# Kernel tuning notes

Measured on AMD Instinct MI355X. Metric: run time of the kernel, lower is better.

## Reference

```python
import jax, jax.numpy as jnp
import numpy as np

B, S, D, H, E, P, TOP_K = 8, 4096, 512, 2048, 8, 16, 2


def setup_inputs() -> dict:
    key = jax.random.key(0)
    ks = jax.random.split(key, 7)
    x = jax.random.normal(ks[0], (B, S, D), dtype=jnp.float32)
    pattern_ids = jax.random.randint(ks[1], (B,), 0, P)
    # router params (init per module: std 0.01 content, std 0.1 pattern bias)
    Wr = 0.01 * jax.random.normal(ks[2], (D, E), dtype=jnp.float32)
    Wp = 0.1 * jax.random.normal(ks[3], (P, E), dtype=jnp.float32)
    # per-expert SwiGLU FFN weights (stacked): w1, w3: [E,D,H], w2: [E,H,D]
    W1 = jax.random.normal(ks[4], (E, D, H), dtype=jnp.float32) / np.float32(np.sqrt(D))
    W2 = jax.random.normal(ks[5], (E, H, D), dtype=jnp.float32) / np.float32(np.sqrt(H))
    W3 = jax.random.normal(ks[6], (E, D, H), dtype=jnp.float32) / np.float32(np.sqrt(D))
    return {"x": x, "pattern_ids": pattern_ids, "Wr": Wr, "Wp": Wp, "W1": W1, "W2": W2, "W3": W3}


def reference(x, pattern_ids, Wr, Wp, W1, W2, W3):
    num_experts = W1.shape[0]
    num_patterns = Wp.shape[0]
    # ---- pattern-aware router ----
    # content logits + per-batch pattern bias broadcast over seq
    logits = jnp.einsum('bsd,de->bse', x, Wr) + Wp[pattern_ids][:, None, :]  # [B,S,E]
    top_w, top_i = jax.lax.top_k(logits, TOP_K)           # [B,S,K]
    gates = jax.nn.softmax(top_w, axis=-1)                # softmax over the top-k logits
    # ---- expert dispatch / combine (loop over small fixed expert count) ----
    y = jnp.zeros_like(x)
    for e in range(num_experts):
        # combined gate weight for expert e per token (0 if not selected)
        w_e = jnp.sum(gates * (top_i == e), axis=-1)      # [B,S]
        h = jnp.einsum('bsd,dh->bsh', x, W1[e]) * jax.nn.silu(jnp.einsum('bsd,dh->bsh', x, W3[e]))
        y = y + w_e[..., None] * jnp.einsum('bsh,hd->bsd', h, W2[e])
    # ---- auxiliary losses ----
    probs = jax.nn.softmax(logits, axis=-1)
    router_z_loss = jnp.mean(jnp.square(logits)) * 0.001
    balance_loss = jnp.mean(jnp.square(probs.mean(axis=(0, 1)) - 1.0 / num_experts))
    Pn = jax.nn.softmax(Wp, axis=-1)
    sim = Pn @ Pn.T
    specialization_loss = jnp.mean(sim * (1.0 - jnp.eye(num_patterns, dtype=sim.dtype))) * 0.1
    return (y, router_z_loss, balance_loss, specialization_loss)
```

## Files before the change

### kernel.cpp

```cpp
#include <hip/hip_runtime.h>
#include <hip/hip_bf16.h>
#include <math.h>


#define B_ 8
#define S_ 4096
#define D_ 512
#define H_ 2048
#define HH (H_ / 2)
#define E_ 8
#define P_ 16
#define NTOK (B_ * S_)
#define NPAIR (NTOK * 2)

typedef __bf16 bf16;
typedef __bf16 bf16x8 __attribute__((ext_vector_type(8)));
typedef float f32x4 __attribute__((ext_vector_type(4)));

#define OFF_GATES 256
#define OFF_LIST (OFF_GATES + NPAIR * 4)
#define OFF_XBF (OFF_LIST + E_ * NTOK * 4)
#define OFF_W13T (OFF_XBF + (size_t)NTOK * D_ * 2)
#define OFF_W2T (OFF_W13T + (size_t)E_ * 2 * H_ * D_ * 2)
#define OFF_HBUF (OFF_W2T + (size_t)E_ * D_ * H_ * 2)
#define WS_NEEDED (OFF_HBUF + (size_t)NPAIR * HH * 2)

__device__ __forceinline__ void gl16(const bf16* g, bf16* l) {
  __builtin_amdgcn_global_load_lds((const __attribute__((address_space(1))) unsigned int*)g,
                                   (__attribute__((address_space(3))) unsigned int*)l, 16, 0, 0);
}

__global__ __launch_bounds__(256) void router_kernel(
    const float* __restrict__ x, const int* __restrict__ pids,
    const float* __restrict__ Wr, const float* __restrict__ Wp,
    bf16* __restrict__ xbf, float* __restrict__ gates, int* __restrict__ lists,
    int* __restrict__ counts, float* __restrict__ probSum, float* __restrict__ zSum) {
  __shared__ float xs[32 * 516];
  __shared__ float wr_s[E_ * 516];
  __shared__ float wp_s[E_];
  __shared__ float probAcc[E_];
  __shared__ float zAcc;
  __shared__ int lcnt[E_], lbase[E_];
  __shared__ float lg_s[32][E_ + 1];

  const int tid = threadIdx.x;
  const int tok0 = blockIdx.x * 32;

#pragma unroll
  for (int rep = 0; rep < (D_ * E_) / 256; ++rep) {
    int flat = rep * 256 + tid;
    wr_s[(flat & 7) * 516 + (flat >> 3)] = Wr[flat];
  }
  if (tid < E_) {
    wp_s[tid] = Wp[pids[tok0 >> 12] * E_ + tid];
    probAcc[tid] = 0.f;
    lcnt[tid] = 0;
  }
  if (tid == 0) zAcc = 0.f;

  const float4* x4 = (const float4*)(x + (size_t)tok0 * D_);
#pragma unroll
  for (int rep = 0; rep < 16; ++rep) {
    int idx = rep * 256 + tid;
    float4 v = x4[idx];
    int t = idx >> 7;
    int d = (idx & 127) * 4;
    *(float4*)(xs + t * 516 + d) = v;
    union { unsigned short u[4]; uint2 qq; } pk;
    pk.u[0] = __builtin_bit_cast(unsigned short, (bf16)v.x);
    pk.u[1] = __builtin_bit_cast(unsigned short, (bf16)v.y);
    pk.u[2] = __builtin_bit_cast(unsigned short, (bf16)v.z);
    pk.u[3] = __builtin_bit_cast(unsigned short, (bf16)v.w);
    *(uint2*)(xbf + (size_t)tok0 * D_ + (size_t)idx * 4) = pk.qq;
  }
  __syncthreads();

  const int t = tid >> 3, e = tid & 7;
  const int lane = tid & 63;
  {
    float a0 = 0.f, a1 = 0.f, a2 = 0.f, a3 = 0.f;
    const float* xr = xs + t * 516;
    const float* wr = wr_s + e * 516;
#pragma unroll 8
    for (int d = 0; d < D_; d += 4) {
      float4 xv = *(const float4*)(xr + d);
      float4 wv = *(const float4*)(wr + d);
      a0 += xv.x * wv.x;
      a1 += xv.y * wv.y;
      a2 += xv.z * wv.z;
      a3 += xv.w * wv.w;
    }
    lg_s[t][e] = (a0 + a1) + (a2 + a3) + wp_s[e];
  }
  __syncthreads();

  float v[E_];
#pragma unroll
  for (int k = 0; k < E_; ++k) v[k] = lg_s[t][k];
  const float lg = v[e];
  float m = v[0];
#pragma unroll
  for (int k = 1; k < E_; ++k) m = fmaxf(m, v[k]);
  float s = 0.f;
#pragma unroll
  for (int k = 0; k < E_; ++k) s += expf(v[k] - m);
  float prob = expf(lg - m) / s;
  float z = lg * lg;
  int i1 = 0;
  float v1 = v[0];
#pragma unroll
  for (int k = 1; k < E_; ++k)
    if (v[k] > v1) { v1 = v[k]; i1 = k; }
  int i2 = -1;
  float v2 = -1e30f;
#pragma unroll
  for (int k = 0; k < E_; ++k)
    if (k != i1 && v[k] > v2) { v2 = v[k]; i2 = k; }

  float p = prob;
  p += __shfl_xor(p, 8);
  p += __shfl_xor(p, 16);
  p += __shfl_xor(p, 32);
  float zz = z;
#pragma unroll
  for (int off = 1; off < 64; off <<= 1) zz += __shfl_xor(zz, off);
  if (lane < 8) atomicAdd(&probAcc[e], p);
  if (lane == 0) atomicAdd(&zAcc, zz);

  int r = (e == i1) ? 0 : ((e == i2) ? 1 : -1);
  int pos = -1;
  if (r >= 0) {
    float ex = expf(v2 - v1);
    float g = (r == 0) ? 1.f / (1.f + ex) : ex / (1.f + ex);
    gates[(tok0 + t) * 2 + r] = g;
    pos = atomicAdd(&lcnt[e], 1);
  }
  __syncthreads();
  if (tid < E_) lbase[tid] = atomicAdd(&counts[tid], lcnt[tid]);
  __syncthreads();
  if (r >= 0) lists[e * NTOK + lbase[e] + pos] = (tok0 + t) * 2 + r;
  if (tid < E_) atomicAdd(&probSum[tid], probAcc[tid]);
  else if (tid == 8) atomicAdd(zSum, zAcc);
}

__global__ __launch_bounds__(256) void transpose_convert(const float* __restrict__ in,
                                                         bf16* __restrict__ out, int R, int C,
                                                         size_t out_estride, int mode) {
  const int e = blockIdx.z;
  const int r0 = blockIdx.y * 64, c0 = blockIdx.x * 64;
  in += (size_t)e * R * C;
  out += (size_t)e * out_estride;
  __shared__ unsigned int lt[64 * 33];

  const int tid = threadIdx.x;
  const int m = tid & 15, qq = tid >> 4;
#pragma unroll
  for (int rep = 0; rep < 2; ++rep) {
    int rp = qq + rep * 16;
    const float4 a = *(const float4*)(in + (size_t)(r0 + rp * 2) * C + c0 + m * 4);
    const float4 b = *(const float4*)(in + (size_t)(r0 + rp * 2 + 1) * C + c0 + m * 4);
#pragma unroll
    for (int j = 0; j < 4; ++j) {
      unsigned short lo = __builtin_bit_cast(unsigned short, (bf16)((&a.x)[j]));
      unsigned short hi = __builtin_bit_cast(unsigned short, (bf16)((&b.x)[j]));
      lt[(m * 4 + j) * 33 + rp] = (unsigned int)lo | ((unsigned int)hi << 16);
    }
  }
  __syncthreads();
  const int c = tid >> 2, dw0 = (tid & 3) * 8;
  unsigned int vv[8];
#pragma unroll
  for (int j = 0; j < 8; ++j) vv[j] = lt[c * 33 + dw0 + j];
  int orow = c0 + c;
  if (mode >= 0) orow = ((orow >> 4) << 5) | (orow & 15) | mode;
  uint4* dst = (uint4*)(out + (size_t)orow * R + r0 + dw0 * 2);
  dst[0] = make_uint4(vv[0], vv[1], vv[2], vv[3]);
  dst[1] = make_uint4(vv[4], vv[5], vv[6], vv[7]);
}

__global__ __launch_bounds__(512, 4) void gemm1_kernel(
    const bf16* __restrict__ xbf, const bf16* __restrict__ W13T,
    const int* __restrict__ counts, const int* __restrict__ lists,
    const float* __restrict__ gates, bf16* __restrict__ hbuf, int half) {
  const int e = (int)blockIdx.z;
  const int count = counts[e];
  const int m0 = blockIdx.y * 128;
  if (m0 >= count) return;
  int hbase = 0;
  for (int j = 0; j < e; ++j) hbase += counts[j];
  const int nb = (int)blockIdx.x;
  const int n0 = nb * 256 + half * (2 * HH);
  const int* list_e = lists + e * NTOK;
  const bf16* Be = W13T + (size_t)e * (2 * H_) * D_;

  __shared__ bf16 sA[2 * 128 * 32];
  __shared__ bf16 sB[2 * 256 * 32];
  __shared__ int stok[128];
  __shared__ float sgate[128];

  const int tid = threadIdx.x;
  if (tid < 128) {
    int rg = m0 + tid;
    int pr = (rg < count) ? list_e[rg] : 0;
    stok[tid] = pr >> 1;
    sgate[tid] = (rg < count) ? gates[pr] : 0.f;
  }
  __syncthreads();

  const int wave = tid >> 6, lane = tid & 63;
  const int rsub = lane >> 2, kq = lane & 3;
  const int scol = (kq ^ ((lane >> 3) & 3)) * 8;
  const int rS = wave * 16 + rsub;
  const bf16* aP0 = xbf + (size_t)stok[rS] * D_ + scol;
  const bf16* bP0 = Be + (size_t)(n0 + rS) * D_ + scol;
  const bf16* bP1 = Be + (size_t)(n0 + 128 + rS) * D_ + scol;
  bf16* lA0 = sA + wave * 512;
  bf16* lB0 = sB + wave * 512;
  bf16* lB1 = sB + (wave + 8) * 512;

  const int wm = wave >> 2, wn = wave & 3;
  const int lm = lane & 15, q = lane >> 4;
  const int rq = (q ^ ((lm >> 1) & 3)) * 8;
  const bf16* aRd = sA + (wm * 64 + lm) * 32 + rq;
  const bf16* bRd = sB + (wn * 64 + lm) * 32 + rq;

  f32x4 acc[4][4] = {};

  gl16(aP0, lA0);
  gl16(bP0, lB0);
  gl16(bP1, lB1);
  __syncthreads();

  int cur = 0;
  for (int t = 1; t < D_ / 32; ++t) {
    const int koff = t * 32;
    const int nxtA = (cur ^ 1) * 4096;
    const int nxtB = (cur ^ 1) * 8192;
    gl16(aP0 + koff, lA0 + nxtA);
    gl16(bP0 + koff, lB0 + nxtB);
    gl16(bP1 + koff, lB1 + nxtB);
    const bf16* aR = aRd + cur * 4096;
    const bf16* bR = bRd + cur * 8192;
    bf16x8 af[4], bf_[4];
#pragma unroll
    for (int i = 0; i < 4; ++i) {
      af[i] = *(const bf16x8*)(aR + i * 512);
      bf_[i] = *(const bf16x8*)(bR + i * 512);
    }
#pragma unroll
    for (int mt = 0; mt < 4; ++mt)
#pragma unroll
      for (int nt = 0; nt < 4; ++nt)
        acc[mt][nt] =
            __builtin_amdgcn_mfma_f32_16x16x32_bf16(af[mt], bf_[nt], acc[mt][nt], 0, 0, 0);
    __syncthreads();
    cur ^= 1;
  }
  {
    const bf16* aR = aRd + cur * 4096;
    const bf16* bR = bRd + cur * 8192;
    bf16x8 af[4], bf_[4];
#pragma unroll
    for (int i = 0; i < 4; ++i) {
      af[i] = *(const bf16x8*)(aR + i * 512);
      bf_[i] = *(const bf16x8*)(bR + i * 512);
    }
#pragma unroll
    for (int mt = 0; mt < 4; ++mt)
#pragma unroll
      for (int nt = 0; nt < 4; ++nt)
        acc[mt][nt] =
            __builtin_amdgcn_mfma_f32_16x16x32_bf16(af[mt], bf_[nt], acc[mt][nt], 0, 0, 0);
  }

  const int hb = nb * 128 + wn * 32;
#pragma unroll
  for (int mt = 0; mt < 4; ++mt) {
#pragma unroll
    for (int u = 0; u < 2; ++u) {
#pragma unroll
      for (int r = 0; r < 4; ++r) {
        int lrow = wm * 64 + mt * 16 + q * 4 + r;
        int grow = m0 + lrow;
        if (grow < count) {
          float v1 = acc[mt][2 * u][r];
          float v3 = acc[mt][2 * u + 1][r];
          float g = v1 * (v3 / (1.f + __expf(-v3))) * sgate[lrow];
          hbuf[(size_t)(hbase + grow) * HH + hb + u * 16 + lm] = (bf16)g;
        }
      }
    }
  }
}

__global__ __launch_bounds__(256, 2) void gemm2_kernel(const bf16* __restrict__ hbuf,
                                                       const bf16* __restrict__ W2T,
                                                       const int* __restrict__ counts,
                                                       const int* __restrict__ lists,
                                                       float* __restrict__ y, int half) {
  const int e = (int)blockIdx.z;
  const int count = counts[e];
  const int m0 = blockIdx.y * 128;
  if (m0 >= count) return;
  int hbase = 0;
  for (int j = 0; j < e; ++j) hbase += counts[j];
  const int n0 = blockIdx.x * 128;
  const int kb = half * HH;
  const bf16* W2e = W2T + (size_t)e * D_ * H_;
  const int* list_e = lists + e * NTOK;

  __shared__ bf16 sA[4 * 128 * 32];
  __shared__ bf16 sB[4 * 128 * 32];
  __shared__ int stok[128];

  const int tid = threadIdx.x;
  if (tid < 128) {
    int rg = m0 + tid;
    stok[tid] = (rg < count) ? (list_e[rg] >> 1) : 0;
  }
  __syncthreads();

  const int wave = tid >> 6, lane = tid & 63;
  const int rsub = lane >> 2, kq = lane & 3;
  const int scol = (kq ^ ((lane >> 3) & 3)) * 8;
  const int rA0 = wave * 16 + rsub, rA1 = 64 + wave * 16 + rsub;
  int ra0 = hbase + m0 + rA0;
  int ra1 = hbase + m0 + rA1;
  if (ra0 >= NPAIR) ra0 = NPAIR - 1;
  if (ra1 >= NPAIR) ra1 = NPAIR - 1;
  const bf16* aP0 = hbuf + (size_t)ra0 * HH + scol;
  const bf16* aP1 = hbuf + (size_t)ra1 * HH + scol;
  const bf16* bP0 = W2e + (size_t)(n0 + rA0) * H_ + kb + scol;
  const bf16* bP1 = W2e + (size_t)(n0 + rA1) * H_ + kb + scol;

  const int wm = wave >> 1, wn = wave & 1;
  const int lm = lane & 15, q = lane >> 4;
  const int rq = (q ^ ((lm >> 1) & 3)) * 8;
  const bf16* aRd = sA + (wm * 64 + lm) * 32 + rq;
  const bf16* bRd = sB + (wn * 64 + lm) * 32 + rq;

  f32x4 acc[4][4] = {};

  auto STAGE = [&](int t, int bi) {
    const int ko = t * 32;
    bf16* ba = sA + bi * 4096;
    bf16* bb = sB + bi * 4096;
    gl16(aP0 + ko, ba + wave * 512);
    gl16(aP1 + ko, ba + (wave + 4) * 512);
    gl16(bP0 + ko, bb + wave * 512);
    gl16(bP1 + ko, bb + (wave + 4) * 512);
  };
  auto COMP = [&](int bi) {
    const bf16* aR = aRd + bi * 4096;
    const bf16* bR = bRd + bi * 4096;
    bf16x8 af[4], bf_[4];
#pragma unroll
    for (int i = 0; i < 4; ++i) {
      af[i] = *(const bf16x8*)(aR + i * 512);
      bf_[i] = *(const bf16x8*)(bR + i * 512);
    }
#pragma unroll
    for (int mt = 0; mt < 4; ++mt)
#pragma unroll
      for (int nt = 0; nt < 4; ++nt)
        acc[mt][nt] =
            __builtin_amdgcn_mfma_f32_16x16x32_bf16(af[mt], bf_[nt], acc[mt][nt], 0, 0, 0);
  };

  const int NT = HH / 32;
  STAGE(0, 0);
  STAGE(1, 1);
  for (int t = 0; t < NT - 2; ++t) {
    STAGE(t + 2, (t + 2) & 3);
    asm volatile("s_waitcnt vmcnt(8) lgkmcnt(0)" ::: "memory");
    __builtin_amdgcn_s_barrier();
    COMP(t & 3);
  }
  asm volatile("s_waitcnt vmcnt(4) lgkmcnt(0)" ::: "memory");
  __builtin_amdgcn_s_barrier();
  COMP((NT - 2) & 3);
  asm volatile("s_waitcnt vmcnt(0) lgkmcnt(0)" ::: "memory");
  __builtin_amdgcn_s_barrier();
  COMP((NT - 1) & 3);

#pragma unroll
  for (int mt = 0; mt < 4; ++mt) {
#pragma unroll
    for (int nt = 0; nt < 4; ++nt) {
#pragma unroll
      for (int r = 0; r < 4; ++r) {
        int lrow = wm * 64 + mt * 16 + q * 4 + r;
        int grow = m0 + lrow;
        if (grow < count) {
          atomicAdd(&y[(size_t)stok[lrow] * D_ + n0 + wn * 64 + nt * 16 + lm], acc[mt][nt][r]);
        }
      }
    }
  }
}

__global__ __launch_bounds__(256) void finalize_kernel(const float* __restrict__ Wp,
                                                       const float* __restrict__ probSum,
                                                       const float* __restrict__ zSum,
                                                       float* __restrict__ out) {
  __shared__ float pn[P_][E_];
  __shared__ float simAcc;
  const int tid = threadIdx.x;
  if (tid == 0) simAcc = 0.f;
  if (tid < P_) {
    float v[E_], m = -1e30f, s = 0.f;
#pragma unroll
    for (int e = 0; e < E_; ++e) {
      v[e] = Wp[tid * E_ + e];
      m = fmaxf(m, v[e]);
    }
#pragma unroll
    for (int e = 0; e < E_; ++e) {
      float ex = expf(v[e] - m);
      pn[tid][e] = ex;
      s += ex;
    }
#pragma unroll
    for (int e = 0; e < E_; ++e) pn[tid][e] /= s;
  }
  __syncthreads();
  {
    int i = tid >> 4, j = tid & 15;
    if (i != j) {
      float d = 0.f;
#pragma unroll
      for (int e = 0; e < E_; ++e) d += pn[i][e] * pn[j][e];
      atomicAdd(&simAcc, d);
    }
  }
  __syncthreads();
  if (tid == 0) {
    out[0] = zSum[0] / (float)(NTOK * E_) * 0.001f;
    float bl = 0.f;
#pragma unroll
    for (int e = 0; e < E_; ++e) {
      float pm = probSum[e] / (float)NTOK - 1.f / (float)E_;
      bl += pm * pm;
    }
    out[1] = bl / (float)E_;
    out[2] = simAcc / (float)(P_ * P_) * 0.1f;
  }
}

extern "C" void kernel_launch(void* const* d_in, const int* in_sizes, int n_in, void* d_out,
                              int out_size, void* d_ws, size_t ws_size, hipStream_t stream) {
  const float* x = (const float*)d_in[0];
  const int* pids = (const int*)d_in[1];
  const float* Wr = (const float*)d_in[2];
  const float* Wp = (const float*)d_in[3];
  const float* W1 = (const float*)d_in[4];
  const float* W2 = (const float*)d_in[5];
  const float* W3 = (const float*)d_in[6];
  float* y = (float*)d_out;

  if (ws_size < WS_NEEDED) return;

  char* ws = (char*)d_ws;
  int* counts = (int*)ws;
  float* probSum = (float*)(ws + 32);
  float* zSum = (float*)(ws + 64);
  float* gates = (float*)(ws + OFF_GATES);
  int* lists = (int*)(ws + OFF_LIST);
  bf16* xbf = (bf16*)(ws + OFF_XBF);
  bf16* W13T = (bf16*)(ws + OFF_W13T);
  bf16* W2T = (bf16*)(ws + OFF_W2T);
  bf16* hbuf = (bf16*)(ws + OFF_HBUF);

  hipMemsetAsync(ws, 0, 256, stream);
  hipMemsetAsync(d_out, 0, (size_t)NTOK * D_ * 4, stream);

  router_kernel<<<dim3(NTOK / 32), 256, 0, stream>>>(x, pids, Wr, Wp, xbf, gates, lists, counts,
                                                     probSum, zSum);
  transpose_convert<<<dim3(H_ / 64, D_ / 64, E_), 256, 0, stream>>>(W1, W13T, D_, H_,
                                                                    (size_t)2 * H_ * D_, 0);
  transpose_convert<<<dim3(H_ / 64, D_ / 64, E_), 256, 0, stream>>>(W3, W13T, D_, H_,
                                                                    (size_t)2 * H_ * D_, 16);
  transpose_convert<<<dim3(D_ / 64, H_ / 64, E_), 256, 0, stream>>>(W2, W2T, H_, D_,
                                                                    (size_t)H_ * D_, -1);

  for (int half = 0; half < 2; ++half) {
    gemm1_kernel<<<dim3((2 * HH) / 256, NTOK / 128, E_), 512, 0, stream>>>(
        xbf, W13T, counts, lists, gates, hbuf, half);
    gemm2_kernel<<<dim3(D_ / 128, NTOK / 128, E_), 256, 0, stream>>>(hbuf, W2T, counts, lists,
                                                                     y, half);
  }
  finalize_kernel<<<1, 256, 0, stream>>>(Wp, probSum, zSum, y + (size_t)NTOK * D_);
}
```

Baseline: 962.9 us.

## Keep full A row-block resident in LDS and stream all gemm1 N-chunks per block

gemm1 now loads a 64-token tile of gathered x (the full K=512) into LDS once, with an XOR swizzle. Each block then loops over all N-chunks of the W1/W3 half, double-buffering B tiles and running a SwiGLU epilogue per 256-column chunk. This removes the repeated gather of x rows across many N blocks and the per-block startup costs. The trade-offs are 64 KB of A in LDS, lower occupancy (launch bounds 4→2), and a much smaller grid with x-dimension 1, which may leave CUs underused.

```diff
diff --git a/kernel.cpp b/kernel.cpp
--- a/kernel.cpp
+++ b/kernel.cpp
@@ -178,118 +178,124 @@
   dst[1] = make_uint4(vv[4], vv[5], vv[6], vv[7]);
 }
 
-__global__ __launch_bounds__(512, 4) void gemm1_kernel(
+__global__ __launch_bounds__(512, 2) void gemm1_kernel(
     const bf16* __restrict__ xbf, const bf16* __restrict__ W13T,
     const int* __restrict__ counts, const int* __restrict__ lists,
     const float* __restrict__ gates, bf16* __restrict__ hbuf, int half) {
   const int e = (int)blockIdx.z;
   const int count = counts[e];
-  const int m0 = blockIdx.y * 128;
+  const int m0 = blockIdx.y * 64;
   if (m0 >= count) return;
   int hbase = 0;
   for (int j = 0; j < e; ++j) hbase += counts[j];
-  const int nb = (int)blockIdx.x;
-  const int n0 = nb * 256 + half * (2 * HH);
   const int* list_e = lists + e * NTOK;
   const bf16* Be = W13T + (size_t)e * (2 * H_) * D_;
 
-  __shared__ bf16 sA[2 * 128 * 32];
-  __shared__ bf16 sB[2 * 256 * 32];
-  __shared__ int stok[128];
-  __shared__ float sgate[128];
+  __shared__ bf16 sA[8 * 4096];
+  __shared__ bf16 sB[2 * 512 * 32];
 
   const int tid = threadIdx.x;
-  if (tid < 128) {
-    int rg = m0 + tid;
-    int pr = (rg < count) ? list_e[rg] : 0;
-    stok[tid] = pr >> 1;
-    sgate[tid] = (rg < count) ? gates[pr] : 0.f;
-  }
-  __syncthreads();
-
   const int wave = tid >> 6, lane = tid & 63;
+  const int lm = lane & 15, q = lane >> 4;
+
+  float gte[4][4];
+#pragma unroll
+  for (int mt = 0; mt < 4; ++mt)
+#pragma unroll
+    for (int r = 0; r < 4; ++r) {
+      int grow = m0 + mt * 16 + q * 4 + r;
+      gte[mt][r] = (grow < count) ? gates[list_e[grow]] : 0.f;
+    }
+
+  const int rA = lane >> 3;
+  const int c16 = lane & 7;
+  {
+    int rowA = m0 + wave * 8 + rA;
+    int prA = (rowA < count) ? list_e[rowA] : 0;
+    const bf16* aSrc = xbf + (size_t)(prA >> 1) * D_ + (c16 ^ rA) * 8;
+    bf16* aDst = sA + wave * 4096;
+#pragma unroll
+    for (int j = 0; j < 8; ++j) gl16(aSrc + j * 64, aDst + j * 512);
+  }
+
   const int rsub = lane >> 2, kq = lane & 3;
   const int scol = (kq ^ ((lane >> 3) & 3)) * 8;
-  const int rS = wave * 16 + rsub;
-  const bf16* aP0 = xbf + (size_t)stok[rS] * D_ + scol;
-  const bf16* bP0 = Be + (size_t)(n0 + rS) * D_ + scol;
-  const bf16* bP1 = Be + (size_t)(n0 + 128 + rS) * D_ + scol;
-  bf16* lA0 = sA + wave * 512;
-  bf16* lB0 = sB + wave * 512;
-  bf16* lB1 = sB + (wave + 8) * 512;
-
-  const int wm = wave >> 2, wn = wave & 3;
-  const int lm = lane & 15, q = lane >> 4;
+  const bf16* bPbase =
+      Be + (size_t)(half * (2 * HH) + wave * 64 + rsub) * D_ + scol;
+  auto STAGE_B = [&](int s, int buf) {
+    int c = s >> 4, t = s & 15;
+    size_t off = (size_t)c * 512 * D_ + t * 32;
+    bf16* d = sB + buf * 16384 + wave * 2048;
+#pragma unroll
+    for (int sl = 0; sl < 4; ++sl) gl16(bPbase + off + (size_t)sl * 16 * D_, d + sl * 512);
+  };
+
+  const int r7 = lm & 7;
+  int aStat[4];
+#pragma unroll
+  for (int mt = 0; mt < 4; ++mt)
+    aStat[mt] = (mt * 2 + (lm >> 3)) * 8192 + (lm & 7) * 128;
   const int rq = (q ^ ((lm >> 1) & 3)) * 8;
-  const bf16* aRd = sA + (wm * 64 + lm) * 32 + rq;
-  const bf16* bRd = sB + (wn * 64 + lm) * 32 + rq;
+  const char* aBase = (const char*)sA;
 
   f32x4 acc[4][4] = {};
 
-  gl16(aP0, lA0);
-  gl16(bP0, lB0);
-  gl16(bP1, lB1);
-  __syncthreads();
-
-  int cur = 0;
-  for (int t = 1; t < D_ / 32; ++t) {
-    const int koff = t * 32;
-    const int nxtA = (cur ^ 1) * 4096;
-    const int nxtB = (cur ^ 1) * 8192;
-    gl16(aP0 + koff, lA0 + nxtA);
-    gl16(bP0 + koff, lB0 + nxtB);
-    gl16(bP1 + koff, lB1 + nxtB);
-    const bf16* aR = aRd + cur * 4096;
-    const bf16* bR = bRd + cur * 8192;
+  auto COMP = [&](int s, int buf) {
+    const int t15 = s & 15;
+    const int c64 = (t15 >> 1) * 1024;
+    const int cc = (t15 * 4 + q) & 7;
     bf16x8 af[4], bf_[4];
 #pragma unroll
-    for (int i = 0; i < 4; ++i) {
-      af[i] = *(const bf16x8*)(aR + i * 512);
-      bf_[i] = *(const bf16x8*)(bR + i * 512);
-    }
+    for (int mt = 0; mt < 4; ++mt)
+      af[mt] = *(const bf16x8*)(aBase + aStat[mt] + c64 + ((cc ^ r7) << 4));
+    const bf16* bR = sB + buf * 16384 + (wave * 64 + lm) * 32 + rq;
+#pragma unroll
+    for (int nt = 0; nt < 4; ++nt) bf_[nt] = *(const bf16x8*)(bR + nt * 512);
 #pragma unroll
     for (int mt = 0; mt < 4; ++mt)
 #pragma unroll
       for (int nt = 0; nt < 4; ++nt)
         acc[mt][nt] =
             __builtin_amdgcn_mfma_f32_16x16x32_bf16(af[mt], bf_[nt], acc[mt][nt], 0, 0, 0);
-    __syncthreads();
-    cur ^= 1;
-  }
-  {
-    const bf16* aR = aRd + cur * 4096;
-    const bf16* bR = bRd + cur * 8192;
-    bf16x8 af[4], bf_[4];
-#pragma unroll
-    for (int i = 0; i < 4; ++i) {
-      af[i] = *(const bf16x8*)(aR + i * 512);
-      bf_[i] = *(const bf16x8*)(bR + i * 512);
-    }
-#pragma unroll
-    for (int mt = 0; mt < 4; ++mt)
-#pragma unroll
-      for (int nt = 0; nt < 4; ++nt)
-        acc[mt][nt] =
-            __builtin_amdgcn_mfma_f32_16x16x32_bf16(af[mt], bf_[nt], acc[mt][nt], 0, 0, 0);
-  }
-
-  const int hb = nb * 128 + wn * 32;
-#pragma unroll
-  for (int mt = 0; mt < 4; ++mt) {
-#pragma unroll
-    for (int u = 0; u < 2; ++u) {
-#pragma unroll
-      for (int r = 0; r < 4; ++r) {
-        int lrow = wm * 64 + mt * 16 + q * 4 + r;
-        int grow = m0 + lrow;
-        if (grow < count) {
-          float v1 = acc[mt][2 * u][r];
-          float v3 = acc[mt][2 * u + 1][r];
-          float g = v1 * (v3 / (1.f + __expf(-v3))) * sgate[lrow];
-          hbuf[(size_t)(hbase + grow) * HH + hb + u * 16 + lm] = (bf16)g;
+  };
+
+  auto EPI = [&](int c) {
+#pragma unroll
+    for (int mt = 0; mt < 4; ++mt) {
+#pragma unroll
+      for (int u = 0; u < 2; ++u) {
+#pragma unroll
+        for (int r = 0; r < 4; ++r) {
+          int grow = m0 + mt * 16 + q * 4 + r;
+          if (grow < count) {
+            float v1 = acc[mt][2 * u][r];
+            float v3 = acc[mt][2 * u + 1][r];
+            float g = v1 * (v3 / (1.f + __expf(-v3))) * gte[mt][r];
+            hbuf[(size_t)(hbase + grow) * HH + c * 256 + wave * 32 + u * 16 + lm] = (bf16)g;
+          }
         }
       }
     }
+#pragma unroll
+    for (int mt = 0; mt < 4; ++mt)
+#pragma unroll
+      for (int nt = 0; nt < 4; ++nt)
+#pragma unroll
+        for (int k2 = 0; k2 < 4; ++k2) acc[mt][nt][k2] = 0.f;
+  };
+
+  STAGE_B(0, 0);
+  __syncthreads();
+
+  for (int ss = 0; ss < 32; ++ss) {
+    const int s0 = 2 * ss, s1 = 2 * ss + 1;
+    STAGE_B(s1, 1);
+    COMP(s0, 0);
+    __syncthreads();
+    if (s1 < 63) STAGE_B(s1 + 1, 0);
+    COMP(s1, 1);
+    __syncthreads();
+    if ((s1 & 15) == 15) EPI(s1 >> 4);
   }
 }
 
@@ -484,8 +490,8 @@
                                                                     (size_t)H_ * D_, -1);
 
   for (int half = 0; half < 2; ++half) {
-    gemm1_kernel<<<dim3((2 * HH) / 256, NTOK / 128, E_), 512, 0, stream>>>(
-        xbf, W13T, counts, lists, gates, hbuf, half);
+    gemm1_kernel<<<dim3(1, NTOK / 64, E_), 512, 0, stream>>>(xbf, W13T, counts, lists, gates,
+                                                             hbuf, half);
     gemm2_kernel<<<dim3(D_ / 128, NTOK / 128, E_), 256, 0, stream>>>(hbuf, W2T, counts, lists,
                                                                      y, half);
   }
```

Measured after the change: 1.232 ms. +28.0%, slower.
